# Kernel tuning notes

Measured on AMD Instinct MI355X. Metric: run time of the kernel, lower is better.

## Reference

```python
import jax, jax.numpy as jnp
import numpy as np

V_SIZE = 128000  # vocab size (v_size init arg)


def setup_inputs() -> dict:
    key = jax.random.key(0)
    k1, k2 = jax.random.split(key)
    # per-position scores -> weighting_scheme (softmax over seq dim)
    w_es = jax.random.normal(k1, (256, 2048), dtype=jnp.float32)
    # instance['x']: token ids in [0, v_size)
    x = jax.random.randint(k2, (256, 2048), 0, V_SIZE, dtype=jnp.int64)
    return {"w_es": w_es, "x": x}


def reference(w_es, x):
    # weighting_scheme(indices, w_es, instance): softmax over sequence positions
    weights = jax.nn.softmax(w_es, axis=-1)          # [B, S]
    B, S = weights.shape
    rows = jnp.arange(B)[:, None]                    # [B, 1] broadcast against [B, S]
    # scatter: w_a[b, x[b, i]] = weights[b, i]  (vectorized index_put)
    w_a = jnp.zeros((B, V_SIZE), dtype=weights.dtype).at[rows, x].set(weights)
    return (w_a, weights)
```

## Files before the change

kernel.cpp:

```cpp
#include <hip/hip_runtime.h>

#define BATCH 256
#define SEQ   2048
#define VOCAB 128000
#define HASH  4096
#define CHUNK 16384

typedef float v4f __attribute__((ext_vector_type(4)));
typedef int   v4i __attribute__((ext_vector_type(4)));

__global__ __launch_bounds__(256)
void softmax_scatter_fused(const float* __restrict__ w_es,
                           const int*   __restrict__ x,
                           float* __restrict__ w_a,
                           float* __restrict__ w_out)
{
    __shared__ int   key [HASH];
    __shared__ int   maxi[HASH];
    __shared__ float val [CHUNK];
    __shared__ float red[8];

    const int r = blockIdx.x;
    const int t = threadIdx.x;
    const int lane = t & 63;
    const int wid  = t >> 6;

    for (int j = t; j < HASH; j += 256) { key[j] = -1; maxi[j] = -1; }

    const float* rowp = w_es + (size_t)r * SEQ;
    const v4f a0 = ((const v4f*)rowp)[t];
    const v4f a1 = ((const v4f*)rowp)[256 + t];

    float m = fmaxf(fmaxf(fmaxf(a0.x, a0.y), fmaxf(a0.z, a0.w)),
                    fmaxf(fmaxf(a1.x, a1.y), fmaxf(a1.z, a1.w)));
    #pragma unroll
    for (int off = 32; off > 0; off >>= 1)
        m = fmaxf(m, __shfl_down(m, off, 64));
    if (lane == 0) red[wid] = m;
    __syncthreads();
    m = fmaxf(fmaxf(red[0], red[1]), fmaxf(red[2], red[3]));

    float e[8];
    e[0] = __expf(a0.x - m); e[1] = __expf(a0.y - m);
    e[2] = __expf(a0.z - m); e[3] = __expf(a0.w - m);
    e[4] = __expf(a1.x - m); e[5] = __expf(a1.y - m);
    e[6] = __expf(a1.z - m); e[7] = __expf(a1.w - m);
    float s = e[0] + e[1] + e[2] + e[3] + e[4] + e[5] + e[6] + e[7];
    #pragma unroll
    for (int off = 32; off > 0; off >>= 1)
        s += __shfl_down(s, off, 64);
    if (lane == 0) red[4 + wid] = s;
    __syncthreads();
    s = red[4] + red[5] + red[6] + red[7];

    const float inv = 1.0f / s;
    float w[8];
    #pragma unroll
    for (int k = 0; k < 8; ++k) w[k] = e[k] * inv;

    float* wrow = w_out + (size_t)r * SEQ;
    v4f w0; w0.x = w[0]; w0.y = w[1]; w0.z = w[2]; w0.w = w[3];
    v4f w1; w1.x = w[4]; w1.y = w[5]; w1.z = w[6]; w1.w = w[7];
    ((v4f*)wrow)[t]       = w0;
    ((v4f*)wrow)[256 + t] = w1;

    const int* xrow = x + (size_t)r * SEQ;
    const v4i x0 = ((const v4i*)xrow)[t];
    const v4i x1 = ((const v4i*)xrow)[256 + t];
    int tok[8] = { x0.x, x0.y, x0.z, x0.w, x1.x, x1.y, x1.z, x1.w };
    int idx[8];
    #pragma unroll
    for (int k = 0; k < 4; ++k) { idx[k] = 4 * t + k; idx[4 + k] = 1024 + 4 * t + k; }

    int slot[8];
    #pragma unroll
    for (int k = 0; k < 8; ++k) {
        unsigned h = (((unsigned)tok[k] * 2654435761u) >> 16) & (HASH - 1);
        int sl = (int)h;
        while (true) {
            int prev = atomicCAS(&key[sl], -1, tok[k]);
            if (prev == -1 || prev == tok[k]) break;
            sl = (sl + 1) & (HASH - 1);
        }
        slot[k] = sl;
        atomicMax(&maxi[sl], idx[k]);
    }
    __syncthreads();

    bool win[8];
    #pragma unroll
    for (int k = 0; k < 8; ++k) win[k] = (maxi[slot[k]] == idx[k]);

    float* warow = w_a + (size_t)r * VOCAB;
    const v4f z4 = (v4f)0.0f;

    for (int base = 0; base < VOCAB; base += CHUNK) {
        const int cnt  = (VOCAB - base < CHUNK) ? (VOCAB - base) : CHUNK;
        const int cnt4 = cnt >> 2;

        for (int j = t; j < cnt4; j += 256)
            ((v4f*)val)[j] = z4;
        __syncthreads();

        #pragma unroll
        for (int k = 0; k < 8; ++k) {
            int v = tok[k] - base;
            if (win[k] && (unsigned)v < (unsigned)cnt)
                val[v] = w[k];
        }
        __syncthreads();

        float* gp = warow + base;
        for (int j = t; j < cnt4; j += 256) {
            v4f v4 = ((const v4f*)val)[j];
            __builtin_nontemporal_store(v4, (v4f*)(gp + 4 * j));
        }
        __syncthreads();
    }
}

extern "C" void kernel_launch(void* const* d_in, const int* in_sizes, int n_in,
                              void* d_out, int out_size, void* d_ws, size_t ws_size,
                              hipStream_t stream) {
    const float* w_es = (const float*)d_in[0];
    const int*   x    = (const int*)d_in[1];

    float* out  = (float*)d_out;
    float* w_a  = out;
    float* w    = out + (size_t)BATCH * VOCAB;

    softmax_scatter_fused<<<BATCH, 256, 0, stream>>>(w_es, x, w_a, w);
}
```

Before: 148.6 us.

## Split each row across eight vocab-chunk blocks and drop the hash table

Launches one block per (row, vocab chunk) instead of one per row, so 2048 blocks share the write of the large w_a output instead of 256. The shared-memory hash table is replaced by a per-chunk array that holds the winning position index via atomicMax. The winning weight then overwrites that index in place, and negative entries are emitted as zero. Each block recomputes the row softmax and rereads x, and the final stores change from nontemporal to regular.

New measurement: 142.6 us. -4.1%, faster.

```diff
diff --git a/kernel.cpp b/kernel.cpp
--- a/kernel.cpp
+++ b/kernel.cpp
@@ -3,29 +3,37 @@
 #define BATCH 256
 #define SEQ   2048
 #define VOCAB 128000
-#define HASH  4096
 #define CHUNK 16384
+#define CPR   8
 
 typedef float v4f __attribute__((ext_vector_type(4)));
 typedef int   v4i __attribute__((ext_vector_type(4)));
 
 __global__ __launch_bounds__(256)
-void softmax_scatter_fused(const float* __restrict__ w_es,
-                           const int*   __restrict__ x,
-                           float* __restrict__ w_a,
-                           float* __restrict__ w_out)
+void softmax_scatter_chunked(const float* __restrict__ w_es,
+                             const int*   __restrict__ x,
+                             float* __restrict__ w_a,
+                             float* __restrict__ w_out)
 {
-    __shared__ int   key [HASH];
-    __shared__ int   maxi[HASH];
-    __shared__ float val [CHUNK];
+    __shared__ int   chunk[CHUNK];
     __shared__ float red[8];
 
-    const int r = blockIdx.x;
+    const int bid = blockIdx.x;
+    const int r = bid >> 3;
+    const int c = bid & (CPR - 1);
+    const int base = c * CHUNK;
+    const int cnt  = (VOCAB - base < CHUNK) ? (VOCAB - base) : CHUNK;
+    const int cnt4 = cnt >> 2;
+
     const int t = threadIdx.x;
     const int lane = t & 63;
     const int wid  = t >> 6;
 
-    for (int j = t; j < HASH; j += 256) { key[j] = -1; maxi[j] = -1; }
+    {
+        const v4i m1 = (v4i)(-1);
+        for (int j = t; j < cnt4; j += 256)
+            ((v4i*)chunk)[j] = m1;
+    }
 
     const float* rowp = w_es + (size_t)r * SEQ;
     const v4f a0 = ((const v4f*)rowp)[t];
@@ -56,13 +64,17 @@
     const float inv = 1.0f / s;
     float w[8];
     #pragma unroll
-    for (int k = 0; k < 8; ++k) w[k] = e[k] * inv;
+    for (int k = 0; k < 8; ++k) w[k] = 0.0f;
+    w[0] = e[0] * inv; w[1] = e[1] * inv; w[2] = e[2] * inv; w[3] = e[3] * inv;
+    w[4] = e[4] * inv; w[5] = e[5] * inv; w[6] = e[6] * inv; w[7] = e[7] * inv;
 
-    float* wrow = w_out + (size_t)r * SEQ;
-    v4f w0; w0.x = w[0]; w0.y = w[1]; w0.z = w[2]; w0.w = w[3];
-    v4f w1; w1.x = w[4]; w1.y = w[5]; w1.z = w[6]; w1.w = w[7];
-    ((v4f*)wrow)[t]       = w0;
-    ((v4f*)wrow)[256 + t] = w1;
+    if (c == 0) {
+        float* wrow = w_out + (size_t)r * SEQ;
+        v4f w0; w0.x = w[0]; w0.y = w[1]; w0.z = w[2]; w0.w = w[3];
+        v4f w1; w1.x = w[4]; w1.y = w[5]; w1.z = w[6]; w1.w = w[7];
+        ((v4f*)wrow)[t]       = w0;
+        ((v4f*)wrow)[256 + t] = w1;
+    }
 
     const int* xrow = x + (size_t)r * SEQ;
     const v4i x0 = ((const v4i*)xrow)[t];
@@ -72,50 +84,33 @@
     #pragma unroll
     for (int k = 0; k < 4; ++k) { idx[k] = 4 * t + k; idx[4 + k] = 1024 + 4 * t + k; }
 
-    int slot[8];
+    int v[8]; bool inr[8];
     #pragma unroll
     for (int k = 0; k < 8; ++k) {
-        unsigned h = (((unsigned)tok[k] * 2654435761u) >> 16) & (HASH - 1);
-        int sl = (int)h;
-        while (true) {
-            int prev = atomicCAS(&key[sl], -1, tok[k]);
-            if (prev == -1 || prev == tok[k]) break;
-            sl = (sl + 1) & (HASH - 1);
-        }
-        slot[k] = sl;
-        atomicMax(&maxi[sl], idx[k]);
+        v[k] = tok[k] - base;
+        inr[k] = (unsigned)v[k] < (unsigned)cnt;
     }
+
+    #pragma unroll
+    for (int k = 0; k < 8; ++k)
+        if (inr[k]) atomicMax(&chunk[v[k]], idx[k]);
     __syncthreads();
 
-    bool win[8];
     #pragma unroll
-    for (int k = 0; k < 8; ++k) win[k] = (maxi[slot[k]] == idx[k]);
+    for (int k = 0; k < 8; ++k)
+        if (inr[k] && chunk[v[k]] == idx[k])
+            ((float*)chunk)[v[k]] = w[k];
+    __syncthreads();
 
-    float* warow = w_a + (size_t)r * VOCAB;
-    const v4f z4 = (v4f)0.0f;
-
-    for (int base = 0; base < VOCAB; base += CHUNK) {
-        const int cnt  = (VOCAB - base < CHUNK) ? (VOCAB - base) : CHUNK;
-        const int cnt4 = cnt >> 2;
-
-        for (int j = t; j < cnt4; j += 256)
-            ((v4f*)val)[j] = z4;
-        __syncthreads();
-
-        #pragma unroll
-        for (int k = 0; k < 8; ++k) {
-            int v = tok[k] - base;
-            if (win[k] && (unsigned)v < (unsigned)cnt)
-                val[v] = w[k];
-        }
-        __syncthreads();
-
-        float* gp = warow + base;
-        for (int j = t; j < cnt4; j += 256) {
-            v4f v4 = ((const v4f*)val)[j];
-            __builtin_nontemporal_store(v4, (v4f*)(gp + 4 * j));
-        }
-        __syncthreads();
+    float* gp = w_a + (size_t)r * VOCAB + base;
+    for (int j = t; j < cnt4; j += 256) {
+        v4i b = ((const v4i*)chunk)[j];
+        v4f o;
+        o.x = (b.x < 0) ? 0.0f : __int_as_float(b.x);
+        o.y = (b.y < 0) ? 0.0f : __int_as_float(b.y);
+        o.z = (b.z < 0) ? 0.0f : __int_as_float(b.z);
+        o.w = (b.w < 0) ? 0.0f : __int_as_float(b.w);
+        ((v4f*)(gp))[j] = o;
     }
 }
 
@@ -129,5 +124,5 @@
     float* w_a  = out;
     float* w    = out + (size_t)BATCH * VOCAB;
 
-    softmax_scatter_fused<<<BATCH, 256, 0, stream>>>(w_es, x, w_a, w);
+    softmax_scatter_chunked<<<BATCH * CPR, 256, 0, stream>>>(w_es, x, w_a, w);
 }
```

## Split softmax-scatter into row-prep and per-chunk row-build kernels

Applied to the files above, without the earlier changes.

The fused kernel is split into two. The first computes the softmax, resolves duplicate tokens with an LDS hash table (the last position wins) and writes the winning (offset, weight) pairs into per-row, per-chunk buckets in workspace. The second launches one block per (row, chunk), 2048 blocks in total, which zero-fills LDS, scatters its bucket and streams the chunk to w_a. This replaces 256 long-running blocks with many shorter ones to get more parallelism on the 131 MB dense write. In exchange it adds a second launch and a workspace round-trip, drops the nontemporal stores, and relies on a fixed bucket capacity of 512 that would silently truncate a chunk with more winning tokens.

Measured after the change: 146.8 us. About the same (-1.2%).

```diff
diff --git a/kernel.cpp b/kernel.cpp
--- a/kernel.cpp
+++ b/kernel.cpp
@@ -5,19 +5,22 @@
 #define VOCAB 128000
 #define HASH  4096
 #define CHUNK 16384
+#define CPR   8
+#define CAP   512
 
 typedef float v4f __attribute__((ext_vector_type(4)));
 typedef int   v4i __attribute__((ext_vector_type(4)));
 
 __global__ __launch_bounds__(256)
-void softmax_scatter_fused(const float* __restrict__ w_es,
-                           const int*   __restrict__ x,
-                           float* __restrict__ w_a,
-                           float* __restrict__ w_out)
+void rowprep_kernel(const float* __restrict__ w_es,
+                    const int*   __restrict__ x,
+                    float* __restrict__ w_out,
+                    int*   __restrict__ counts,
+                    int2*  __restrict__ pairs)
 {
     __shared__ int   key [HASH];
     __shared__ int   maxi[HASH];
-    __shared__ float val [CHUNK];
+    __shared__ int   cnt [CPR];
     __shared__ float red[8];
 
     const int r = blockIdx.x;
@@ -26,6 +29,7 @@
     const int wid  = t >> 6;
 
     for (int j = t; j < HASH; j += 256) { key[j] = -1; maxi[j] = -1; }
+    if (t < CPR) cnt[t] = 0;
 
     const float* rowp = w_es + (size_t)r * SEQ;
     const v4f a0 = ((const v4f*)rowp)[t];
@@ -55,8 +59,8 @@
 
     const float inv = 1.0f / s;
     float w[8];
-    #pragma unroll
-    for (int k = 0; k < 8; ++k) w[k] = e[k] * inv;
+    w[0] = e[0] * inv; w[1] = e[1] * inv; w[2] = e[2] * inv; w[3] = e[3] * inv;
+    w[4] = e[4] * inv; w[5] = e[5] * inv; w[6] = e[6] * inv; w[7] = e[7] * inv;
 
     float* wrow = w_out + (size_t)r * SEQ;
     v4f w0; w0.x = w[0]; w0.y = w[1]; w0.z = w[2]; w0.w = w[3];
@@ -87,36 +91,52 @@
     }
     __syncthreads();
 
-    bool win[8];
     #pragma unroll
-    for (int k = 0; k < 8; ++k) win[k] = (maxi[slot[k]] == idx[k]);
+    for (int k = 0; k < 8; ++k) {
+        if (maxi[slot[k]] == idx[k]) {
+            int c   = tok[k] >> 14;
+            int pos = atomicAdd(&cnt[c], 1);
+            if (pos < CAP)
+                pairs[(size_t)(r * CPR + c) * CAP + pos] =
+                    make_int2(tok[k] & (CHUNK - 1), __float_as_int(w[k]));
+        }
+    }
+    __syncthreads();
+    if (t < CPR) counts[r * CPR + t] = min(cnt[t], CAP);
+}
 
-    float* warow = w_a + (size_t)r * VOCAB;
-    const v4f z4 = (v4f)0.0f;
+__global__ __launch_bounds__(256)
+void buildrow_kernel(const int*  __restrict__ counts,
+                     const int2* __restrict__ pairs,
+                     float* __restrict__ w_a)
+{
+    __shared__ float val[CHUNK];
 
-    for (int base = 0; base < VOCAB; base += CHUNK) {
-        const int cnt  = (VOCAB - base < CHUNK) ? (VOCAB - base) : CHUNK;
-        const int cnt4 = cnt >> 2;
+    const int bid = blockIdx.x;
+    const int r = bid >> 3;
+    const int c = bid & (CPR - 1);
+    const int base = c * CHUNK;
+    const int cnt  = (VOCAB - base < CHUNK) ? (VOCAB - base) : CHUNK;
+    const int cnt4 = cnt >> 2;
+    const int t = threadIdx.x;
 
-        for (int j = t; j < cnt4; j += 256)
-            ((v4f*)val)[j] = z4;
-        __syncthreads();
+    const v4f z = (v4f)0.0f;
+    for (int j = t; j < cnt4; j += 256)
+        ((v4f*)val)[j] = z;
 
-        #pragma unroll
-        for (int k = 0; k < 8; ++k) {
-            int v = tok[k] - base;
-            if (win[k] && (unsigned)v < (unsigned)cnt)
-                val[v] = w[k];
-        }
-        __syncthreads();
+    const int n = counts[r * CPR + c];
+    __syncthreads();
 
-        float* gp = warow + base;
-        for (int j = t; j < cnt4; j += 256) {
-            v4f v4 = ((const v4f*)val)[j];
-            __builtin_nontemporal_store(v4, (v4f*)(gp + 4 * j));
-        }
-        __syncthreads();
+    const int2* pp = pairs + (size_t)(r * CPR + c) * CAP;
+    for (int p = t; p < n; p += 256) {
+        int2 pr = pp[p];
+        val[pr.x] = __int_as_float(pr.y);
     }
+    __syncthreads();
+
+    float* gp = w_a + (size_t)r * VOCAB + base;
+    for (int j = t; j < cnt4; j += 256)
+        ((v4f*)gp)[j] = ((const v4f*)val)[j];
 }
 
 extern "C" void kernel_launch(void* const* d_in, const int* in_sizes, int n_in,
@@ -129,5 +149,9 @@
     float* w_a  = out;
     float* w    = out + (size_t)BATCH * VOCAB;
 
-    softmax_scatter_fused<<<BATCH, 256, 0, stream>>>(w_es, x, w_a, w);
+    int*  counts = (int*)d_ws;
+    int2* pairs  = (int2*)((char*)d_ws + BATCH * CPR * sizeof(int));
+
+    rowprep_kernel <<<BATCH,       256, 0, stream>>>(w_es, x, w, counts, pairs);
+    buildrow_kernel<<<BATCH * CPR, 256, 0, stream>>>(counts, pairs, w_a);
 }
```
